# Kernel tuning notes

Hardware: AMD Instinct MI355X
Metric: run time of the kernel (lower is better)

## Reference

```python
import jax, jax.numpy as jnp
import numpy as np

B, T = 32, 64
C, H, W = 1, 32, 32
A, E, D, S, HID = 2, 64, 128, 32, 128
K, STRIDE, PAD = 4, 2, 1
FEAT = 64 * 4 * 4  # conv stack output: 64 channels at 4x4


def _lin(x, w, b):
    return x @ w.T + b


def _conv(x, w, b):
    y = jax.lax.conv_general_dilated(x, w, (STRIDE, STRIDE), [(PAD, PAD)] * 2,
                                     dimension_numbers=('NCHW', 'OIHW', 'NCHW'))
    return y + b[None, :, None, None]


def _deconv(x, w, b):
    # torch ConvTranspose2d(w: (in_c,out_c,k,k), stride=2, pad=1) as dilated conv
    w_ = jnp.flip(w, (2, 3)).transpose(1, 0, 2, 3)
    p = K - 1 - PAD
    y = jax.lax.conv_general_dilated(x, w_, (1, 1), [(p, p)] * 2,
                                     lhs_dilation=(STRIDE, STRIDE),
                                     dimension_numbers=('NCHW', 'OIHW', 'NCHW'))
    return y + b[None, :, None, None]


def _mlp(x, w1, b1, w2, b2, w3, b3):
    h = jax.nn.elu(_lin(x, w1, b1))
    h = jax.nn.elu(_lin(h, w2, b2))
    out = _lin(h, w3, b3)
    return out[..., :S], jnp.clip(out[..., S:], -5.0, 2.0)


def _gru(x, h, wih, whh, bih, bhh):
    # torch nn.GRUCell semantics
    gi = x @ wih.T + bih
    gh = h @ whh.T + bhh
    ir, iz, inn = jnp.split(gi, 3, -1)
    hr, hz, hn = jnp.split(gh, 3, -1)
    r = jax.nn.sigmoid(ir + hr)
    u = jax.nn.sigmoid(iz + hz)
    n = jnp.tanh(inn + r * hn)
    return (1.0 - u) * n + u * h


def setup_inputs():
    keys = iter(jax.random.split(jax.random.key(0), 64))

    def p(shape, fan):
        return jax.random.normal(next(keys), shape, jnp.float32) / np.sqrt(fan)

    return dict(
        obs=jax.random.normal(next(keys), (B, T, C, H, W), jnp.float32),
        actions=jax.random.normal(next(keys), (B, T, A), jnp.float32),
        noise=jax.random.normal(next(keys), (T, B, S), jnp.float32),
        enc_w1=p((32, C, K, K), C * K * K), enc_b1=jnp.zeros(32),
        enc_w2=p((64, 32, K, K), 32 * K * K), enc_b2=jnp.zeros(64),
        enc_w3=p((64, 64, K, K), 64 * K * K), enc_b3=jnp.zeros(64),
        enc_pw=p((E, FEAT), FEAT), enc_pb=jnp.zeros(E),
        dec_pw=p((FEAT, D + S), D + S), dec_pb=jnp.zeros(FEAT),
        dec_w1=p((64, 64, K, K), 64 * K * K), dec_b1=jnp.zeros(64),
        dec_w2=p((64, 32, K, K), 64 * K * K), dec_b2=jnp.zeros(32),
        dec_w3=p((32, C, K, K), 32 * K * K), dec_b3=jnp.zeros(C),
        gru_wih=p((3 * D, S + A), D), gru_whh=p((3 * D, D), D),
        gru_bih=jnp.zeros(3 * D), gru_bhh=jnp.zeros(3 * D),
        pri_w1=p((HID, D + A), D + A), pri_b1=jnp.zeros(HID),
        pri_w2=p((HID, HID), HID), pri_b2=jnp.zeros(HID),
        pri_w3=p((2 * S, HID), HID), pri_b3=jnp.zeros(2 * S),
        pos_w1=p((HID, D + E), D + E), pos_b1=jnp.zeros(HID),
        pos_w2=p((HID, HID), HID), pos_b2=jnp.zeros(HID),
        pos_w3=p((2 * S, HID), HID), pos_b3=jnp.zeros(2 * S),
    )


def reference(obs, actions, noise, enc_w1, enc_b1, enc_w2, enc_b2, enc_w3, enc_b3,
              enc_pw, enc_pb, dec_pw, dec_pb, dec_w1, dec_b1, dec_w2, dec_b2,
              dec_w3, dec_b3, gru_wih, gru_whh, gru_bih, gru_bhh,
              pri_w1, pri_b1, pri_w2, pri_b2, pri_w3, pri_b3,
              pos_w1, pos_b1, pos_w2, pos_b2, pos_w3, pos_b3):
    Bq, Tq = obs.shape[:2]
    # --- CNN encoder over all frames at once ---
    x = obs.reshape(Bq * Tq, C, H, W)
    x = jax.nn.relu(_conv(x, enc_w1, enc_b1))
    x = jax.nn.relu(_conv(x, enc_w2, enc_b2))
    x = jax.nn.relu(_conv(x, enc_w3, enc_b3))
    embed = _lin(x.reshape(Bq * Tq, -1), enc_pw, enc_pb).reshape(Bq, Tq, E)

    # --- sequential RSSM core (use_posterior=True path) ---
    def step(h, inp):
        a, e_t, eps = inp
        pm, pls = _mlp(jnp.concatenate([h, e_t], -1),
                       pos_w1, pos_b1, pos_w2, pos_b2, pos_w3, pos_b3)
        z = pm + jnp.exp(pls) * eps
        prm, prls = _mlp(jnp.concatenate([h, a], -1),
                         pri_w1, pri_b1, pri_w2, pri_b2, pri_w3, pri_b3)
        h_new = _gru(jnp.concatenate([z, a], -1), h, gru_wih, gru_whh, gru_bih, gru_bhh)
        return h_new, (z, prm, prls, pm, pls, h)  # h = pre-update (used for decode)

    h0 = jnp.zeros((Bq, D), obs.dtype)
    h_final, (zs, prm, prls, pm, pls, hs) = jax.lax.scan(
        step, h0, (actions.swapaxes(0, 1), embed.swapaxes(0, 1), noise))

    # --- batched decode of all (h_t, z_t); same math as per-step decode ---
    hz = jnp.concatenate([hs, zs], -1).reshape(Tq * Bq, D + S)
    y = _lin(hz, dec_pw, dec_pb).reshape(Tq * Bq, 64, 4, 4)
    y = jax.nn.relu(_deconv(y, dec_w1, dec_b1))
    y = jax.nn.relu(_deconv(y, dec_w2, dec_b2))
    y = jax.nn.sigmoid(_deconv(y, dec_w3, dec_b3))
    recons = y.reshape(Tq, Bq, C, H, W).swapaxes(0, 1)

    tb = lambda t: t.swapaxes(0, 1)  # (T,B,.) -> (B,T,.)
    return (recons, tb(zs), tb(prm), tb(prls), tb(pm), tb(pls), h_final)
```

## Files before the change

kernel.cpp:

```cpp
#include <hip/hip_runtime.h>
#include <math.h>

#define NB 32
#define NT 64
#define NF 2048

#define OUT_ZS    2097152
#define OUT_PRM   (OUT_ZS + 65536)
#define OUT_PRLS  (OUT_PRM + 65536)
#define OUT_PM    (OUT_PRLS + 65536)
#define OUT_PLS   (OUT_PM + 65536)
#define OUT_HF    (OUT_PLS + 65536)

#define WS_HS    27394048
#define WS_ENCT  27656192
#define WS_DECT  27721728
#define WS_WP1H  27885568
#define WS_WP2   27893760
#define WS_WP3   27901952
#define WS_WWHH  27906048
#define WS_WIHZ  27930624
#define WS_QW1T  27936768
#define WS_QW2T  27953408
#define WS_QW3T  27969792
#define WS_PW1T  27977984
#define WS_WIHT  28002560
#define WS_WC2   16777216
#define WS_WC3   (WS_WC2 + 16384)
#define WS_WD1   (WS_WC3 + 32768)
#define WS_WD2   (WS_WD1 + 32768)
#define WS_POSL1E 25165824
#define WS_GIA    (WS_POSL1E + 262144)

typedef __attribute__((ext_vector_type(8))) short short8;
typedef __attribute__((ext_vector_type(4))) float floatx4;
typedef _Float16 __attribute__((ext_vector_type(2))) half2v;
union U4S8 { uint4 u; short8 s; };
__device__ __forceinline__ short8 u2s(uint4 u) { U4S8 x; x.u = u; return x.s; }
__device__ __forceinline__ float eluf(float a) { return (a > 0.f) ? a : expm1f(a); }
__device__ __forceinline__ float sigm(float a) { return 1.f / (1.f + expf(-a)); }
__device__ __forceinline__ unsigned short f2bf(float f) {
  unsigned int u = __float_as_uint(f);
  u += 0x7fffu + ((u >> 16) & 1u);
  return (unsigned short)(u >> 16);
}
__device__ __forceinline__ unsigned short f2h(float f) {
  _Float16 h = (_Float16)f;
  return __builtin_bit_cast(unsigned short, h);
}
__device__ __forceinline__ float dotp8(uint4 u, const float* __restrict__ x) {
  float4 x0 = *reinterpret_cast<const float4*>(x);
  float4 x1 = *reinterpret_cast<const float4*>(x + 4);
  float acc;
  acc  = __uint_as_float(u.x << 16) * x0.x;
  acc += __uint_as_float(u.x & 0xffff0000u) * x0.y;
  acc += __uint_as_float(u.y << 16) * x0.z;
  acc += __uint_as_float(u.y & 0xffff0000u) * x0.w;
  acc += __uint_as_float(u.z << 16) * x1.x;
  acc += __uint_as_float(u.z & 0xffff0000u) * x1.y;
  acc += __uint_as_float(u.w << 16) * x1.z;
  acc += __uint_as_float(u.w & 0xffff0000u) * x1.w;
  return acc;
}

union U4H2 { uint4 u; half2v h[4]; };
__device__ __forceinline__ void dot8h(uint4 w, uint4 x,
                                      float& a0, float& a1, float& a2, float& a3) {
  U4H2 W; W.u = w;
  U4H2 X; X.u = x;
#if __has_builtin(__builtin_amdgcn_fdot2)
  a0 = __builtin_amdgcn_fdot2(W.h[0], X.h[0], a0, false);
  a1 = __builtin_amdgcn_fdot2(W.h[1], X.h[1], a1, false);
  a2 = __builtin_amdgcn_fdot2(W.h[2], X.h[2], a2, false);
  a3 = __builtin_amdgcn_fdot2(W.h[3], X.h[3], a3, false);
#else
  a0 = fmaf((float)W.h[0][0], (float)X.h[0][0], a0);
  a0 = fmaf((float)W.h[0][1], (float)X.h[0][1], a0);
  a1 = fmaf((float)W.h[1][0], (float)X.h[1][0], a1);
  a1 = fmaf((float)W.h[1][1], (float)X.h[1][1], a1);
  a2 = fmaf((float)W.h[2][0], (float)X.h[2][0], a2);
  a2 = fmaf((float)W.h[2][1], (float)X.h[2][1], a2);
  a3 = fmaf((float)W.h[3][0], (float)X.h[3][0], a3);
  a3 = fmaf((float)W.h[3][1], (float)X.h[3][1], a3);
#endif
}

struct PP { const float* src; void* dst; int n; int mode; int A; int B; };
struct PPAll { PP m[16]; };

__global__ __launch_bounds__(256) void k_prep(PPAll a) {
  PP p = a.m[blockIdx.y];
  for (int i = blockIdx.x * 256 + threadIdx.x; i < p.n; i += gridDim.x * 256) {
    if (p.mode == 10) {
      const int r = i / p.B, c = i - r * p.B;
      ((float*)p.dst)[c * p.A + r] = p.src[i];
    } else {
      float v;
      if (p.mode == 0) v = p.src[i];
      else if (p.mode == 1) v = p.src[(i >> 7) * 192 + (i & 127)];
      else if (p.mode == 2) v = p.src[(i >> 5) * 34 + (i & 31)];
      else {
        const int ab = p.A * p.B;
        const int t = i / ab, rem = i - t * ab;
        const int oc = rem / p.B, ic = rem - oc * p.B;
        v = (p.mode == 3) ? p.src[(oc * p.B + ic) * 16 + t]
                          : p.src[(ic * p.A + oc) * 16 + t];
      }
      ((unsigned short*)p.dst)[i] = (p.mode <= 2) ? f2h(v) : f2bf(v);
    }
  }
}

__global__ __launch_bounds__(256, 2) void k_enc(
    const float* __restrict__ obs, const float* __restrict__ act,
    const float* __restrict__ w1, const float* __restrict__ b1,
    const unsigned short* __restrict__ wc2, const float* __restrict__ b2,
    const unsigned short* __restrict__ wc3, const float* __restrict__ b3,
    const float* __restrict__ encT, const float* __restrict__ encb,
    const float* __restrict__ pw1T, const float* __restrict__ pb1,
    const float* __restrict__ wihT, const float* __restrict__ bih,
    float* __restrict__ posl1e, float* __restrict__ gia) {
  const int f = blockIdx.x, tid = threadIdx.x;
  const int w = tid >> 6, l = tid & 63, q = l >> 4, n = l & 15;
  __shared__ float sIn1[32 * 33];
  __shared__ float sW1[512];
  __shared__ float sB1[32];
  __shared__ __align__(16) unsigned short sIn2[18 * 18 * 40];
  __shared__ __align__(16) unsigned short sIn3[10 * 10 * 72];
  __shared__ __align__(16) float sXe[1024];
  __shared__ float sP[256];
  __shared__ float sE[64];
  __shared__ float sA2[2];

  {
    const float* in = obs + (size_t)f * 1024;
    for (int i = tid; i < 1024; i += 256) sIn1[(i >> 5) * 33 + (i & 31)] = in[i];
    for (int i = tid; i < 512; i += 256) sW1[i] = w1[i];
    if (tid < 32) sB1[tid] = b1[tid];
    if (tid < 2) sA2[tid] = act[(size_t)f * 2 + tid];
    unsigned int* z2 = (unsigned int*)sIn2;
    for (int i = tid; i < 18 * 18 * 40 / 2; i += 256) z2[i] = 0u;
    unsigned int* z3 = (unsigned int*)sIn3;
    for (int i = tid; i < 10 * 10 * 72 / 2; i += 256) z3[i] = 0u;
  }
  __syncthreads();
  for (int r = tid; r < 512; r += 256) {
    const int oc = r >> 4, oy = r & 15;
    float acc[16];
    const float bv = sB1[oc];
#pragma unroll
    for (int j = 0; j < 16; j++) acc[j] = bv;
#pragma unroll
    for (int ky = 0; ky < 4; ky++) {
      const int iy = 2 * oy + ky - 1;
      if (iy < 0 || iy >= 32) continue;
#pragma unroll
      for (int kx = 0; kx < 4; kx++) {
        const float wv = sW1[oc * 16 + ky * 4 + kx];
#pragma unroll
        for (int j = 0; j < 16; j++) {
          const int ix = 2 * j + kx - 1;
          if (ix >= 0 && ix < 32) acc[j] += wv * sIn1[iy * 33 + ix];
        }
      }
    }
#pragma unroll
    for (int j = 0; j < 16; j++)
      sIn2[((oy + 1) * 18 + (j + 1)) * 40 + oc] = f2bf(fmaxf(acc[j], 0.f));
  }
  __syncthreads();
  {
    int base[4];
#pragma unroll
    for (int nt = 0; nt < 4; nt++) {
      const int px = nt * 16 + n, oy = px >> 3, ox = px & 7;
      base[nt] = ((2 * oy + 1) * 18 + (2 * ox + 1)) * 40 + q * 8;
    }
    floatx4 acc[4];
#pragma unroll
    for (int nt = 0; nt < 4; nt++) acc[nt] = (floatx4){0.f, 0.f, 0.f, 0.f};
    uint4 af[16];
#pragma unroll
    for (int t = 0; t < 16; t++)
      af[t] = *reinterpret_cast<const uint4*>(wc2 + (size_t)(t * 64 + w * 16 + n) * 32 + q * 8);
#pragma unroll
    for (int t = 0; t < 16; t++) {
      const int toff = ((t / 4 - 1) * 18 + (t % 4 - 1)) * 40;
#pragma unroll
      for (int nt = 0; nt < 4; nt++) {
        uint4 bf = *reinterpret_cast<const uint4*>(&sIn2[base[nt] + toff]);
        acc[nt] = __builtin_amdgcn_mfma_f32_16x16x32_bf16(u2s(af[t]), u2s(bf), acc[nt], 0, 0, 0);
      }
    }
    float b4[4];
#pragma unroll
    for (int r = 0; r < 4; r++) b4[r] = b2[w * 16 + q * 4 + r];
    __syncthreads();
#pragma unroll
    for (int nt = 0; nt < 4; nt++) {
      const int px = nt * 16 + n, oy = px >> 3, ox = px & 7;
#pragma unroll
      for (int r = 0; r < 4; r++)
        sIn3[((oy + 1) * 10 + (ox + 1)) * 72 + (w * 16 + q * 4 + r)] =
            f2bf(fmaxf(acc[nt][r] + b4[r], 0.f));
    }
  }
  __syncthreads();
  {
    const int oy = n >> 2, ox = n & 3;
    const int ibase = ((2 * oy + 1) * 10 + (2 * ox + 1)) * 72 + q * 8;
    floatx4 acc = (floatx4){0.f, 0.f, 0.f, 0.f};
    for (int ks = 0; ks < 2; ks++) {
      uint4 af[16];
#pragma unroll
      for (int t = 0; t < 16; t++)
        af[t] = *reinterpret_cast<const uint4*>(
            wc3 + (size_t)(t * 64 + w * 16 + n) * 64 + ks * 32 + q * 8);
#pragma unroll
      for (int t = 0; t < 16; t++) {
        const int toff = ((t / 4 - 1) * 10 + (t % 4 - 1)) * 72 + ks * 32;
        uint4 bf = *reinterpret_cast<const uint4*>(&sIn3[ibase + toff]);
        acc = __builtin_amdgcn_mfma_f32_16x16x32_bf16(u2s(af[t]), u2s(bf), acc, 0, 0, 0);
      }
    }
#pragma unroll
    for (int r = 0; r < 4; r++) {
      const int ch = w * 16 + q * 4 + r;
      sXe[ch * 16 + n] = fmaxf(acc[r] + b3[ch], 0.f);
    }
  }
  __syncthreads();
  {
    const int o = tid & 63, s = tid >> 6;
    float acc = 0.f;
    const int k0 = s * 256;
    for (int k = k0; k < k0 + 256; k++) acc += encT[k * 64 + o] * sXe[k];
    sP[tid] = acc;
  }
  __syncthreads();
  if (tid < 64)
    sE[tid] = sP[tid] + sP[tid + 64] + sP[tid + 128] + sP[tid + 192] + encb[tid];
  __syncthreads();
  if (tid < 128) {
    float a = pb1[tid];
    for (int k = 0; k < 64; k++) a += pw1T[(128 + k) * 128 + tid] * sE[k];
    posl1e[(size_t)f * 128 + tid] = a;
  } else {
#pragma unroll
    for (int jj = 0; jj < 3; jj++) {
      const int j = (tid - 128) + jj * 128;
      gia[(size_t)f * 384 + j] =
          bih[j] + wihT[32 * 384 + j] * sA2[0] + wihT[33 * 384 + j] * sA2[1];
    }
  }
}

__global__ __launch_bounds__(512, 2) void k_rssm4(
    const float* __restrict__ posl1e, const float* __restrict__ gia,
    const float* __restrict__ noise,
    const unsigned short* __restrict__ wp1h, const unsigned short* __restrict__ wp2,
    const unsigned short* __restrict__ wp3, const unsigned short* __restrict__ wwhh,
    const unsigned short* __restrict__ wihz,
    const float* __restrict__ pb2, const float* __restrict__ pb3,
    const float* __restrict__ bhh,
    float* __restrict__ hs, float* __restrict__ out) {
  const int b = blockIdx.x, tid = threadIdx.x;
  __shared__ __align__(16) _Float16 sHh[128];
  __shared__ __align__(16) _Float16 sL1h[128];
  __shared__ __align__(16) _Float16 sL2h[128];
  __shared__ __align__(16) _Float16 sZh[32];
  __shared__ float sGh[384];
  __shared__ float sPM[64];

  uint4 wA[16];
  {
    const unsigned short* rowA =
        (tid < 128) ? (wp1h + tid * 128) : (wwhh + (size_t)(tid - 128) * 128);
#pragma unroll
    for (int i = 0; i < 16; i++) wA[i] = reinterpret_cast<const uint4*>(rowA)[i];
  }
  uint4 wB[4];
  {
    const unsigned short* rowB = wp2 + (tid >> 2) * 128 + (tid & 3) * 32;
#pragma unroll
    for (int i = 0; i < 4; i++) wB[i] = reinterpret_cast<const uint4*>(rowB)[i];
  }
  uint4 wC[2];
  {
    const unsigned short* rowC = wp3 + (tid >> 3) * 128 + (tid & 7) * 16;
#pragma unroll
    for (int i = 0; i < 2; i++) wC[i] = reinterpret_cast<const uint4*>(rowC)[i];
  }
  uint4 wD[3][4];
  if (tid < 128) {
#pragma unroll
    for (int j = 0; j < 3; j++) {
      const unsigned short* rowD = wihz + (size_t)(tid + 128 * j) * 32;
#pragma unroll
      for (int i = 0; i < 4; i++) wD[j][i] = reinterpret_cast<const uint4*>(rowD)[i];
    }
  }
  const float bhhR = (tid >= 128) ? bhh[tid - 128] : 0.f;
  const float pb2R = pb2[tid >> 2];
  const float pb3mR = (tid < 32) ? pb3[tid] : 0.f;
  const float pb3sR = (tid < 32) ? pb3[tid + 32] : 0.f;

  float h_reg = 0.f;
  float pl1R = 0.f, gaR0 = 0.f, gaR1 = 0.f, gaR2 = 0.f, epsR = 0.f;
  if (tid < 128) {
    pl1R = posl1e[(size_t)(b * 64) * 128 + tid];
    const size_t gb = (size_t)(b * 64) * 384 + tid;
    gaR0 = gia[gb];
    gaR1 = gia[gb + 128];
    gaR2 = gia[gb + 256];
    sHh[tid] = (_Float16)0.f;
    hs[(size_t)b * 128 + tid] = 0.f;
  }
  if (tid < 32) epsR = noise[(size_t)b * 32 + tid];
  __syncthreads();

  for (int t = 0; t < 64; ++t) {
    const int tn = (t < 63) ? t + 1 : 63;
    float pl1N = 0.f, gaN0 = 0.f, gaN1 = 0.f, gaN2 = 0.f, epsN = 0.f;
    if (tid < 128) {
      pl1N = posl1e[(size_t)(b * 64 + tn) * 128 + tid];
      const size_t gb = (size_t)(b * 64 + tn) * 384 + tid;
      gaN0 = gia[gb];
      gaN1 = gia[gb + 128];
      gaN2 = gia[gb + 256];
    }
    if (tid < 32) epsN = noise[(size_t)(tn * 32 + b) * 32 + tid];

    {
      float a0 = 0.f, a1 = 0.f, a2 = 0.f, a3 = 0.f;
      const uint4* xs = reinterpret_cast<const uint4*>(sHh);
#pragma unroll
      for (int g = 0; g < 16; g++) dot8h(wA[g], xs[g], a0, a1, a2, a3);
      const float a = (a0 + a1) + (a2 + a3);
      if (tid < 128) sL1h[tid] = (_Float16)eluf(a + pl1R);
      else sGh[tid - 128] = a + bhhR;
    }
    __syncthreads();
    {
      float a0 = 0.f, a1 = 0.f, a2 = 0.f, a3 = 0.f;
      const uint4* xs = reinterpret_cast<const uint4*>(sL1h) + (tid & 3) * 4;
#pragma unroll
      for (int i = 0; i < 4; i++) dot8h(wB[i], xs[i], a0, a1, a2, a3);
      float p = (a0 + a1) + (a2 + a3);
      p += __shfl_xor(p, 1);
      p += __shfl_xor(p, 2);
      if ((tid & 3) == 0) sL2h[tid >> 2] = (_Float16)eluf(p + pb2R);
    }
    __syncthreads();
    {
      float a0 = 0.f, a1 = 0.f, a2 = 0.f, a3 = 0.f;
      const uint4* xs = reinterpret_cast<const uint4*>(sL2h) + (tid & 7) * 2;
      dot8h(wC[0], xs[0], a0, a1, a2, a3);
      dot8h(wC[1], xs[1], a0, a1, a2, a3);
      float p = (a0 + a1) + (a2 + a3);
      p += __shfl_xor(p, 1);
      p += __shfl_xor(p, 2);
      p += __shfl_xor(p, 4);
      if ((tid & 7) == 0) sPM[tid >> 3] = p;
    }
    __syncthreads();
    if (tid < 32) {
      const float pm = sPM[tid] + pb3mR;
      float pls = sPM[32 + tid] + pb3sR;
      pls = fminf(fmaxf(pls, -5.f), 2.f);
      const float z = pm + expf(pls) * epsR;
      sZh[tid] = (_Float16)z;
      const int o = (b * 64 + t) * 32 + tid;
      out[OUT_ZS + o] = z;
      out[OUT_PM + o] = pm;
      out[OUT_PLS + o] = pls;
    }
    __syncthreads();
    if (tid < 128) {
      float r0 = 0.f, r1 = 0.f, r2 = 0.f, r3 = 0.f;
      float u0 = 0.f, u1 = 0.f, u2 = 0.f, u3 = 0.f;
      float m0 = 0.f, m1 = 0.f, m2 = 0.f, m3 = 0.f;
      const uint4* xs = reinterpret_cast<const uint4*>(sZh);
#pragma unroll
      for (int i = 0; i < 4; i++) {
        const uint4 xv = xs[i];
        dot8h(wD[0][i], xv, r0, r1, r2, r3);
        dot8h(wD[1][i], xv, u0, u1, u2, u3);
        dot8h(wD[2][i], xv, m0, m1, m2, m3);
      }
      const float gr = gaR0 + ((r0 + r1) + (r2 + r3));
      const float gu = gaR1 + ((u0 + u1) + (u2 + u3));
      const float gn = gaR2 + ((m0 + m1) + (m2 + m3));
      const float r = sigm(gr + sGh[tid]);
      const float u = sigm(gu + sGh[128 + tid]);
      const float n = tanhf(gn + r * sGh[256 + tid]);
      const float hn = (1.f - u) * n + u * h_reg;
      h_reg = hn;
      sHh[tid] = (_Float16)hn;
      if (t < 63) hs[(size_t)((t + 1) * 32 + b) * 128 + tid] = hn;
    }
    pl1R = pl1N;
    gaR0 = gaN0;
    gaR1 = gaN1;
    gaR2 = gaN2;
    epsR = epsN;
    __syncthreads();
  }
  if (tid < 128) out[OUT_HF + b * 128 + tid] = h_reg;
}

__global__ __launch_bounds__(128) void k_pri(const float* __restrict__ hs,
    const float* __restrict__ act,
    const float* __restrict__ qw1T, const float* __restrict__ qb1,
    const float* __restrict__ qw2T, const float* __restrict__ qb2,
    const float* __restrict__ qw3T, const float* __restrict__ qb3,
    float* __restrict__ out) {
  __shared__ float sV[128], sW[128];
  __shared__ float sA2[2];
  const int f = blockIdx.x, tid = threadIdx.x;
  const int t = f >> 5, b = f & 31;
  sV[tid] = hs[(size_t)f * 128 + tid];
  if (tid < 2) sA2[tid] = act[(size_t)(b * 64 + t) * 2 + tid];
  __syncthreads();
  {
    float a = qb1[tid];
    for (int k = 0; k < 128; k++) a += qw1T[k * 128 + tid] * sV[k];
    a += qw1T[128 * 128 + tid] * sA2[0] + qw1T[129 * 128 + tid] * sA2[1];
    sW[tid] = eluf(a);
  }
  __syncthreads();
  {
    float a = qb2[tid];
    for (int k = 0; k < 128; k++) a += qw2T[k * 128 + tid] * sW[k];
    sV[tid] = eluf(a);
  }
  __syncthreads();
  if (tid < 64) {
    float a = qb3[tid];
    for (int k = 0; k < 128; k++) a += qw3T[k * 64 + tid] * sV[k];
    const int o = (b * 64 + t) * 32;
    if (tid < 32) out[OUT_PRM + o + tid] = a;
    else out[OUT_PRLS + o + tid - 32] = fminf(fmaxf(a, -5.f), 2.f);
  }
}

__global__ __launch_bounds__(256, 2) void k_dec(
    const float* __restrict__ hs, const float* __restrict__ zs,
    const float* __restrict__ decT, const float* __restrict__ decb,
    const unsigned short* __restrict__ wd1, const float* __restrict__ db1,
    const unsigned short* __restrict__ wd2, const float* __restrict__ db2,
    const float* __restrict__ w3, const float* __restrict__ b3,
    float* __restrict__ out) {
  const int f = blockIdx.x, tid = threadIdx.x;
  const int w = tid >> 6, l = tid & 63, q = l >> 4, n = l & 15;
  const int t = f >> 5, b = f & 31;
  __shared__ float sX[160];
  __shared__ __align__(16) unsigned short sInD1[6 * 6 * 72];
  __shared__ __align__(16) unsigned short sInD2[10 * 10 * 72];
  __shared__ float sInD3[32 * 16 * 17];
  __shared__ float sW3[32 * 16 * 2];

  if (tid < 128) sX[tid] = hs[(size_t)f * 128 + tid];
  else if (tid < 160) sX[tid] = zs[(size_t)(b * 64 + t) * 32 + (tid - 128)];
  {
    unsigned int* z1 = (unsigned int*)sInD1;
    for (int i = tid; i < 6 * 6 * 72 / 2; i += 256) z1[i] = 0u;
    unsigned int* z2 = (unsigned int*)sInD2;
    for (int i = tid; i < 10 * 10 * 72 / 2; i += 256) z2[i] = 0u;
    for (int s = tid; s < 512; s += 256) {
      const int icc = s >> 4, tap = s & 15;
      sW3[(icc * 16 + tap) * 2] = w3[s];
    }
  }
  __syncthreads();
  {
    float acc[4];
#pragma unroll
    for (int i = 0; i < 4; i++) acc[i] = decb[i * 256 + tid];
    for (int k = 0; k < 160; k++) {
      const float xv = sX[k];
#pragma unroll
      for (int i = 0; i < 4; i++) acc[i] += decT[k * 1024 + i * 256 + tid] * xv;
    }
#pragma unroll
    for (int i = 0; i < 4; i++) {
      const int o = i * 256 + tid, c = o >> 4, px = o & 15;
      const int Y = px >> 2, X = px & 3;
      sInD1[((Y + 1) * 6 + (X + 1)) * 72 + c] = f2bf(acc[i]);
    }
  }
  __syncthreads();
  {
    const int Y = n >> 2, X = n & 3;
    const int ibase = ((Y + 1) * 6 + (X + 1)) * 72 + q * 8;
    float b4[4];
#pragma unroll
    for (int r = 0; r < 4; r++) b4[r] = db1[w * 16 + q * 4 + r];
#pragma unroll
    for (int c = 0; c < 4; c++) {
      const int cy = c >> 1, cx = c & 1;
      floatx4 acc = (floatx4){0.f, 0.f, 0.f, 0.f};
      for (int ks = 0; ks < 2; ks++) {
        uint4 af[4];
#pragma unroll
        for (int tt = 0; tt < 4; tt++) {
          const int t2 = tt >> 1, t3 = tt & 1;
          const int ky = ((cy + 1) & 1) + 2 * t2, kx = ((cx + 1) & 1) + 2 * t3;
          af[tt] = *reinterpret_cast<const uint4*>(
              wd1 + (size_t)((ky * 4 + kx) * 64 + w * 16 + n) * 64 + ks * 32 + q * 8);
        }
#pragma unroll
        for (int tt = 0; tt < 4; tt++) {
          const int t2 = tt >> 1, t3 = tt & 1;
          const int toff = ((cy - t2) * 6 + (cx - t3)) * 72 + ks * 32;
          uint4 bf = *reinterpret_cast<const uint4*>(&sInD1[ibase + toff]);
          acc = __builtin_amdgcn_mfma_f32_16x16x32_bf16(u2s(af[tt]), u2s(bf), acc, 0, 0, 0);
        }
      }
      const int oy = 2 * Y + cy, ox = 2 * X + cx;
#pragma unroll
      for (int r = 0; r < 4; r++)
        sInD2[((oy + 1) * 10 + (ox + 1)) * 72 + (w * 16 + q * 4 + r)] =
            f2bf(fmaxf(acc[r] + b4[r], 0.f));
    }
  }
  __syncthreads();
  {
    const int px = w * 16 + n;
    const int Y = px >> 3, X = px & 7;
    const int ibase = ((Y + 1) * 10 + (X + 1)) * 72 + q * 8;
    float b4[2][4];
#pragma unroll
    for (int mi = 0; mi < 2; mi++)
#pragma unroll
      for (int r = 0; r < 4; r++) b4[mi][r] = db2[mi * 16 + q * 4 + r];
#pragma unroll
    for (int c = 0; c < 4; c++) {
      const int cy = c >> 1, cx = c & 1;
      floatx4 acc[2];
      acc[0] = (floatx4){0.f, 0.f, 0.f, 0.f};
      acc[1] = (floatx4){0.f, 0.f, 0.f, 0.f};
      for (int ks = 0; ks < 2; ks++) {
        uint4 af[2][4];
#pragma unroll
        for (int mi = 0; mi < 2; mi++)
#pragma unroll
          for (int tt = 0; tt < 4; tt++) {
            const int t2 = tt >> 1, t3 = tt & 1;
            const int ky = ((cy + 1) & 1) + 2 * t2, kx = ((cx + 1) & 1) + 2 * t3;
            af[mi][tt] = *reinterpret_cast<const uint4*>(
                wd2 + (size_t)((ky * 4 + kx) * 32 + mi * 16 + n) * 64 + ks * 32 + q * 8);
          }
#pragma unroll
        for (int tt = 0; tt < 4; tt++) {
          const int t2 = tt >> 1, t3 = tt & 1;
          const int toff = ((cy - t2) * 10 + (cx - t3)) * 72 + ks * 32;
          uint4 bf = *reinterpret_cast<const uint4*>(&sInD2[ibase + toff]);
#pragma unroll
          for (int mi = 0; mi < 2; mi++)
            acc[mi] = __builtin_amdgcn_mfma_f32_16x16x32_bf16(u2s(af[mi][tt]), u2s(bf),
                                                              acc[mi], 0, 0, 0);
        }
      }
      const int oy = 2 * Y + cy, ox = 2 * X + cx;
#pragma unroll
      for (int mi = 0; mi < 2; mi++)
#pragma unroll
        for (int r = 0; r < 4; r++) {
          const int oc = mi * 16 + q * 4 + r;
          sInD3[oc * 272 + oy * 17 + ox] = fmaxf(acc[mi][r] + b4[mi][r], 0.f);
        }
    }
  }
  __syncthreads();
  {
    const int oy = tid >> 3;
    const int rem2 = tid & 7;
    const int cpar = rem2 >> 2, qq = rem2 & 3;
    const int py = (oy + 1) & 1, pc = (cpar + 1) & 1;
    float acc[4];
    const float bv = b3[0];
#pragma unroll
    for (int j = 0; j < 4; j++) acc[j] = bv;
    for (int icc = 0; icc < 32; icc++) {
      const float* inb = &sInD3[icc * 272];
      const float* wb = &sW3[icc * 32];
#pragma unroll
      for (int t2 = 0; t2 < 2; t2++) {
        const int ky = py + 2 * t2;
        const int iy = (oy + 1 - ky) >> 1;
        if (iy < 0 || iy >= 16) continue;
        const float* row = inb + iy * 17;
#pragma unroll
        for (int t3 = 0; t3 < 2; t3++) {
          const int kx = pc + 2 * t3;
          const int ixb = (cpar + 1 - kx) >> 1;
          const float wv = wb[(ky * 4 + kx) * 2];
#pragma unroll
          for (int j = 0; j < 4; j++) {
            const int ix = ixb + qq * 4 + j;
            if (ix >= 0 && ix < 16) acc[j] += wv * row[ix];
          }
        }
      }
    }
    const int fo = b * 64 + t;
    float* yf = out + (size_t)fo * 1024;
#pragma unroll
    for (int j = 0; j < 4; j++)
      yf[oy * 32 + (cpar + 2 * (qq * 4 + j))] = 1.f / (1.f + expf(-acc[j]));
  }
}

extern "C" void kernel_launch(void* const* d_in, const int* in_sizes, int n_in,
                              void* d_out, int out_size, void* d_ws, size_t ws_size,
                              hipStream_t stream) {
  const float* obs = (const float*)d_in[0];
  const float* actions = (const float*)d_in[1];
  const float* noise = (const float*)d_in[2];
  const float* enc_w1 = (const float*)d_in[3];
  const float* enc_b1 = (const float*)d_in[4];
  const float* enc_w2 = (const float*)d_in[5];
  const float* enc_b2 = (const float*)d_in[6];
  const float* enc_w3 = (const float*)d_in[7];
  const float* enc_b3 = (const float*)d_in[8];
  const float* enc_pw = (const float*)d_in[9];
  const float* enc_pb = (const float*)d_in[10];
  const float* dec_pw = (const float*)d_in[11];
  const float* dec_pb = (const float*)d_in[12];
  const float* dec_w1 = (const float*)d_in[13];
  const float* dec_b1 = (const float*)d_in[14];
  const float* dec_w2 = (const float*)d_in[15];
  const float* dec_b2 = (const float*)d_in[16];
  const float* dec_w3 = (const float*)d_in[17];
  const float* dec_b3 = (const float*)d_in[18];
  const float* gru_wih = (const float*)d_in[19];
  const float* gru_whh = (const float*)d_in[20];
  const float* gru_bih = (const float*)d_in[21];
  const float* gru_bhh = (const float*)d_in[22];
  const float* pri_w1 = (const float*)d_in[23];
  const float* pri_b1 = (const float*)d_in[24];
  const float* pri_w2 = (const float*)d_in[25];
  const float* pri_b2 = (const float*)d_in[26];
  const float* pri_w3 = (const float*)d_in[27];
  const float* pri_b3 = (const float*)d_in[28];
  const float* pos_w1 = (const float*)d_in[29];
  const float* pos_b1 = (const float*)d_in[30];
  const float* pos_w2 = (const float*)d_in[31];
  const float* pos_b2 = (const float*)d_in[32];
  const float* pos_w3 = (const float*)d_in[33];
  const float* pos_b3 = (const float*)d_in[34];

  float* out = (float*)d_out;
  float* ws = (float*)d_ws;
  float* HS = ws + WS_HS;
  float* POSL1E = ws + WS_POSL1E;
  float* GIA = ws + WS_GIA;
  unsigned short* WP1H = (unsigned short*)(ws + WS_WP1H);
  unsigned short* WP2 = (unsigned short*)(ws + WS_WP2);
  unsigned short* WP3 = (unsigned short*)(ws + WS_WP3);
  unsigned short* WWHH = (unsigned short*)(ws + WS_WWHH);
  unsigned short* WIHZ = (unsigned short*)(ws + WS_WIHZ);
  unsigned short* WC2 = (unsigned short*)(ws + WS_WC2);
  unsigned short* WC3 = (unsigned short*)(ws + WS_WC3);
  unsigned short* WD1 = (unsigned short*)(ws + WS_WD1);
  unsigned short* WD2 = (unsigned short*)(ws + WS_WD2);

  PPAll pp;
  pp.m[0]  = {enc_pw, ws + WS_ENCT, 64 * 1024, 10, 64, 1024};
  pp.m[1]  = {dec_pw, ws + WS_DECT, 1024 * 160, 10, 1024, 160};
  pp.m[2]  = {pri_w1, ws + WS_QW1T, 128 * 130, 10, 128, 130};
  pp.m[3]  = {pri_w2, ws + WS_QW2T, 128 * 128, 10, 128, 128};
  pp.m[4]  = {pri_w3, ws + WS_QW3T, 64 * 128, 10, 64, 128};
  pp.m[5]  = {pos_w1, ws + WS_PW1T, 128 * 192, 10, 128, 192};
  pp.m[6]  = {gru_wih, ws + WS_WIHT, 384 * 34, 10, 384, 34};
  pp.m[7]  = {pos_w1, WP1H, 128 * 128, 1, 0, 0};
  pp.m[8]  = {pos_w2, WP2, 128 * 128, 0, 0, 0};
  pp.m[9]  = {pos_w3, WP3, 64 * 128, 0, 0, 0};
  pp.m[10] = {gru_whh, WWHH, 384 * 128, 0, 0, 0};
  pp.m[11] = {gru_wih, WIHZ, 384 * 32, 2, 0, 0};
  pp.m[12] = {enc_w2, WC2, 16 * 64 * 32, 3, 64, 32};
  pp.m[13] = {enc_w3, WC3, 16 * 64 * 64, 3, 64, 64};
  pp.m[14] = {dec_w1, WD1, 16 * 64 * 64, 4, 64, 64};
  pp.m[15] = {dec_w2, WD2, 16 * 32 * 64, 4, 32, 64};
  hipLaunchKernelGGL(k_prep, dim3(32, 16), dim3(256), 0, stream, pp);

  k_enc<<<NF, 256, 0, stream>>>(obs, actions, enc_w1, enc_b1, WC2, enc_b2,
                                WC3, enc_b3, ws + WS_ENCT, enc_pb,
                                ws + WS_PW1T, pos_b1, ws + WS_WIHT, gru_bih,
                                POSL1E, GIA);

  k_rssm4<<<NB, 512, 0, stream>>>(POSL1E, GIA, noise, WP1H, WP2, WP3, WWHH, WIHZ,
                                  pos_b2, pos_b3, gru_bhh, HS, out);
  k_pri<<<NF, 128, 0, stream>>>(HS, actions, ws + WS_QW1T, pri_b1,
                                ws + WS_QW2T, pri_b2, ws + WS_QW3T, pri_b3, out);

  k_dec<<<NF, 256, 0, stream>>>(HS, out + OUT_ZS, ws + WS_DECT, dec_pb,
                                WD1, dec_b1, WD2, dec_b2, dec_w3, dec_b3, out);
}
```

Baseline: 508.7 us.

## Use fp16 packed dot products in decoder projection and final deconv

The decoder's dense projection now reads fp16 weights, repacked by the prep kernel into a k-quad interleaved layout, and uses fdot2 instead of fp32 FMAs. The final deconvolution stores its input activations and weights in fp16, channel-innermost, in shared memory and computes with dot8h. This cuts shared memory use and lets launch bounds ask for 4 blocks per SM instead of 2. It lowers global and LDS bandwidth per block and raises occupancy, at the cost of fp16 rounding of activations and weights.

```diff
diff --git a/kernel.cpp b/kernel.cpp
--- a/kernel.cpp
+++ b/kernel.cpp
@@ -48,19 +48,15 @@
   _Float16 h = (_Float16)f;
   return __builtin_bit_cast(unsigned short, h);
 }
-__device__ __forceinline__ float dotp8(uint4 u, const float* __restrict__ x) {
-  float4 x0 = *reinterpret_cast<const float4*>(x);
-  float4 x1 = *reinterpret_cast<const float4*>(x + 4);
-  float acc;
-  acc  = __uint_as_float(u.x << 16) * x0.x;
-  acc += __uint_as_float(u.x & 0xffff0000u) * x0.y;
-  acc += __uint_as_float(u.y << 16) * x0.z;
-  acc += __uint_as_float(u.y & 0xffff0000u) * x0.w;
-  acc += __uint_as_float(u.z << 16) * x1.x;
-  acc += __uint_as_float(u.z & 0xffff0000u) * x1.y;
-  acc += __uint_as_float(u.w << 16) * x1.z;
-  acc += __uint_as_float(u.w & 0xffff0000u) * x1.w;
-  return acc;
+union UH2 { unsigned int u; half2v h; };
+__device__ __forceinline__ half2v u2h(unsigned int u) { UH2 x; x.u = u; return x.h; }
+
+__device__ __forceinline__ float fdot2w(half2v a, half2v b, float c) {
+#if __has_builtin(__builtin_amdgcn_fdot2)
+  return __builtin_amdgcn_fdot2(a, b, c, false);
+#else
+  return fmaf((float)a[0], (float)b[0], fmaf((float)a[1], (float)b[1], c));
+#endif
 }
 
 union U4H2 { uint4 u; half2v h[4]; };
@@ -68,21 +64,10 @@
                                       float& a0, float& a1, float& a2, float& a3) {
   U4H2 W; W.u = w;
   U4H2 X; X.u = x;
-#if __has_builtin(__builtin_amdgcn_fdot2)
-  a0 = __builtin_amdgcn_fdot2(W.h[0], X.h[0], a0, false);
-  a1 = __builtin_amdgcn_fdot2(W.h[1], X.h[1], a1, false);
-  a2 = __builtin_amdgcn_fdot2(W.h[2], X.h[2], a2, false);
-  a3 = __builtin_amdgcn_fdot2(W.h[3], X.h[3], a3, false);
-#else
-  a0 = fmaf((float)W.h[0][0], (float)X.h[0][0], a0);
-  a0 = fmaf((float)W.h[0][1], (float)X.h[0][1], a0);
-  a1 = fmaf((float)W.h[1][0], (float)X.h[1][0], a1);
-  a1 = fmaf((float)W.h[1][1], (float)X.h[1][1], a1);
-  a2 = fmaf((float)W.h[2][0], (float)X.h[2][0], a2);
-  a2 = fmaf((float)W.h[2][1], (float)X.h[2][1], a2);
-  a3 = fmaf((float)W.h[3][0], (float)X.h[3][0], a3);
-  a3 = fmaf((float)W.h[3][1], (float)X.h[3][1], a3);
-#endif
+  a0 = fdot2w(W.h[0], X.h[0], a0);
+  a1 = fdot2w(W.h[1], X.h[1], a1);
+  a2 = fdot2w(W.h[2], X.h[2], a2);
+  a3 = fdot2w(W.h[3], X.h[3], a3);
 }
 
 struct PP { const float* src; void* dst; int n; int mode; int A; int B; };
@@ -99,14 +84,17 @@
       if (p.mode == 0) v = p.src[i];
       else if (p.mode == 1) v = p.src[(i >> 7) * 192 + (i & 127)];
       else if (p.mode == 2) v = p.src[(i >> 5) * 34 + (i & 31)];
-      else {
+      else if (p.mode == 5) {
+        const int kq = i >> 12, o = (i >> 2) & 1023, kl = (i >> 1) & 1, h = i & 1;
+        v = p.src[o * 160 + kq * 4 + kl * 2 + h];
+      } else {
         const int ab = p.A * p.B;
         const int t = i / ab, rem = i - t * ab;
         const int oc = rem / p.B, ic = rem - oc * p.B;
         v = (p.mode == 3) ? p.src[(oc * p.B + ic) * 16 + t]
                           : p.src[(ic * p.A + oc) * 16 + t];
       }
-      ((unsigned short*)p.dst)[i] = (p.mode <= 2) ? f2h(v) : f2bf(v);
+      ((unsigned short*)p.dst)[i] = (p.mode <= 2 || p.mode == 5) ? f2h(v) : f2bf(v);
     }
   }
 }
@@ -444,9 +432,9 @@
   }
 }
 
-__global__ __launch_bounds__(256, 2) void k_dec(
+__global__ __launch_bounds__(256, 4) void k_dec(
     const float* __restrict__ hs, const float* __restrict__ zs,
-    const float* __restrict__ decT, const float* __restrict__ decb,
+    const unsigned short* __restrict__ decTh, const float* __restrict__ decb,
     const unsigned short* __restrict__ wd1, const float* __restrict__ db1,
     const unsigned short* __restrict__ wd2, const float* __restrict__ db2,
     const float* __restrict__ w3, const float* __restrict__ b3,
@@ -454,39 +442,46 @@
   const int f = blockIdx.x, tid = threadIdx.x;
   const int w = tid >> 6, l = tid & 63, q = l >> 4, n = l & 15;
   const int t = f >> 5, b = f & 31;
-  __shared__ float sX[160];
+  __shared__ __align__(16) _Float16 sXh[160];
   __shared__ __align__(16) unsigned short sInD1[6 * 6 * 72];
   __shared__ __align__(16) unsigned short sInD2[10 * 10 * 72];
-  __shared__ float sInD3[32 * 16 * 17];
-  __shared__ float sW3[32 * 16 * 2];
-
-  if (tid < 128) sX[tid] = hs[(size_t)f * 128 + tid];
-  else if (tid < 160) sX[tid] = zs[(size_t)(b * 64 + t) * 32 + (tid - 128)];
+  __shared__ __align__(16) _Float16 sInD3h[16 * 16 * 32];
+  __shared__ __align__(16) _Float16 sW3h[16 * 32];
+
+  if (tid < 128) sXh[tid] = (_Float16)hs[(size_t)f * 128 + tid];
+  else if (tid < 160) sXh[tid] = (_Float16)zs[(size_t)(b * 64 + t) * 32 + (tid - 128)];
   {
     unsigned int* z1 = (unsigned int*)sInD1;
     for (int i = tid; i < 6 * 6 * 72 / 2; i += 256) z1[i] = 0u;
     unsigned int* z2 = (unsigned int*)sInD2;
     for (int i = tid; i < 10 * 10 * 72 / 2; i += 256) z2[i] = 0u;
     for (int s = tid; s < 512; s += 256) {
-      const int icc = s >> 4, tap = s & 15;
-      sW3[(icc * 16 + tap) * 2] = w3[s];
-    }
-  }
-  __syncthreads();
-  {
-    float acc[4];
-#pragma unroll
-    for (int i = 0; i < 4; i++) acc[i] = decb[i * 256 + tid];
-    for (int k = 0; k < 160; k++) {
-      const float xv = sX[k];
-#pragma unroll
-      for (int i = 0; i < 4; i++) acc[i] += decT[k * 1024 + i * 256 + tid] * xv;
+      const int tap = s >> 5, icc = s & 31;
+      sW3h[s] = (_Float16)w3[icc * 16 + tap];
+    }
+  }
+  __syncthreads();
+  {
+    float acA[4] = {0.f, 0.f, 0.f, 0.f};
+    float acB[4] = {0.f, 0.f, 0.f, 0.f};
+    const uint2* dT = reinterpret_cast<const uint2*>(decTh);
+    const unsigned int* xh = reinterpret_cast<const unsigned int*>(sXh);
+#pragma unroll 2
+    for (int kq = 0; kq < 40; kq++) {
+      const half2v x0 = u2h(xh[2 * kq]);
+      const half2v x1 = u2h(xh[2 * kq + 1]);
+#pragma unroll
+      for (int i = 0; i < 4; i++) {
+        const uint2 wv = dT[kq * 1024 + i * 256 + tid];
+        acA[i] = fdot2w(u2h(wv.x), x0, acA[i]);
+        acB[i] = fdot2w(u2h(wv.y), x1, acB[i]);
+      }
     }
 #pragma unroll
     for (int i = 0; i < 4; i++) {
       const int o = i * 256 + tid, c = o >> 4, px = o & 15;
       const int Y = px >> 2, X = px & 3;
-      sInD1[((Y + 1) * 6 + (X + 1)) * 72 + c] = f2bf(acc[i]);
+      sInD1[((Y + 1) * 6 + (X + 1)) * 72 + c] = f2bf(acA[i] + acB[i] + decb[o]);
     }
   }
   __syncthreads();
@@ -564,12 +559,16 @@
       }
       const int oy = 2 * Y + cy, ox = 2 * X + cx;
 #pragma unroll
-      for (int mi = 0; mi < 2; mi++)
-#pragma unroll
-        for (int r = 0; r < 4; r++) {
-          const int oc = mi * 16 + q * 4 + r;
-          sInD3[oc * 272 + oy * 17 + ox] = fmaxf(acc[mi][r] + b4[mi][r], 0.f);
-        }
+      for (int mi = 0; mi < 2; mi++) {
+        const unsigned int lo =
+            (unsigned int)f2h(fmaxf(acc[mi][0] + b4[mi][0], 0.f)) |
+            ((unsigned int)f2h(fmaxf(acc[mi][1] + b4[mi][1], 0.f)) << 16);
+        const unsigned int hi =
+            (unsigned int)f2h(fmaxf(acc[mi][2] + b4[mi][2], 0.f)) |
+            ((unsigned int)f2h(fmaxf(acc[mi][3] + b4[mi][3], 0.f)) << 16);
+        *reinterpret_cast<uint2*>(&sInD3h[(oy * 16 + ox) * 32 + mi * 16 + q * 4]) =
+            make_uint2(lo, hi);
+      }
     }
   }
   __syncthreads();
@@ -578,29 +577,30 @@
     const int rem2 = tid & 7;
     const int cpar = rem2 >> 2, qq = rem2 & 3;
     const int py = (oy + 1) & 1, pc = (cpar + 1) & 1;
-    float acc[4];
+    float acc[4] = {0.f, 0.f, 0.f, 0.f};
     const float bv = b3[0];
 #pragma unroll
-    for (int j = 0; j < 4; j++) acc[j] = bv;
-    for (int icc = 0; icc < 32; icc++) {
-      const float* inb = &sInD3[icc * 272];
-      const float* wb = &sW3[icc * 32];
-#pragma unroll
-      for (int t2 = 0; t2 < 2; t2++) {
-        const int ky = py + 2 * t2;
-        const int iy = (oy + 1 - ky) >> 1;
-        if (iy < 0 || iy >= 16) continue;
-        const float* row = inb + iy * 17;
-#pragma unroll
-        for (int t3 = 0; t3 < 2; t3++) {
-          const int kx = pc + 2 * t3;
-          const int ixb = (cpar + 1 - kx) >> 1;
-          const float wv = wb[(ky * 4 + kx) * 2];
-#pragma unroll
-          for (int j = 0; j < 4; j++) {
-            const int ix = ixb + qq * 4 + j;
-            if (ix >= 0 && ix < 16) acc[j] += wv * row[ix];
-          }
+    for (int u2 = 0; u2 < 2; u2++) {
+      const int ky = py + 2 * u2;
+      const int iy = (oy + 1 - ky) >> 1;
+      if (iy < 0 || iy >= 16) continue;
+#pragma unroll
+      for (int u3 = 0; u3 < 2; u3++) {
+        const int kx = pc + 2 * u3;
+        const int ixb = (cpar + 1 - kx) >> 1;
+        const uint4* wv = reinterpret_cast<const uint4*>(&sW3h[(ky * 4 + kx) * 32]);
+        const uint4 w0 = wv[0], w1 = wv[1], w2 = wv[2], w3v = wv[3];
+#pragma unroll
+        for (int j = 0; j < 4; j++) {
+          const int ix = ixb + qq * 4 + j;
+          if (ix < 0 || ix >= 16) continue;
+          const uint4* xp = reinterpret_cast<const uint4*>(&sInD3h[(iy * 16 + ix) * 32]);
+          float a0 = 0.f, a1 = 0.f, a2 = 0.f, a3 = 0.f;
+          dot8h(w0, xp[0], a0, a1, a2, a3);
+          dot8h(w1, xp[1], a0, a1, a2, a3);
+          dot8h(w2, xp[2], a0, a1, a2, a3);
+          dot8h(w3v, xp[3], a0, a1, a2, a3);
+          acc[j] += (a0 + a1) + (a2 + a3);
         }
       }
     }
@@ -608,7 +608,7 @@
     float* yf = out + (size_t)fo * 1024;
 #pragma unroll
     for (int j = 0; j < 4; j++)
-      yf[oy * 32 + (cpar + 2 * (qq * 4 + j))] = 1.f / (1.f + expf(-acc[j]));
+      yf[oy * 32 + (cpar + 2 * (qq * 4 + j))] = 1.f / (1.f + expf(-(acc[j] + bv)));
   }
 }
 
@@ -665,10 +665,11 @@
   unsigned short* WC3 = (unsigned short*)(ws + WS_WC3);
   unsigned short* WD1 = (unsigned short*)(ws + WS_WD1);
   unsigned short* WD2 = (unsigned short*)(ws + WS_WD2);
+  unsigned short* DECTH = (unsigned short*)(ws + WS_DECT);
 
   PPAll pp;
   pp.m[0]  = {enc_pw, ws + WS_ENCT, 64 * 1024, 10, 64, 1024};
-  pp.m[1]  = {dec_pw, ws + WS_DECT, 1024 * 160, 10, 1024, 160};
+  pp.m[1]  = {dec_pw, DECTH, 160 * 1024, 5, 0, 0};
   pp.m[2]  = {pri_w1, ws + WS_QW1T, 128 * 130, 10, 128, 130};
   pp.m[3]  = {pri_w2, ws + WS_QW2T, 128 * 128, 10, 128, 128};
   pp.m[4]  = {pri_w3, ws + WS_QW3T, 64 * 128, 10, 64, 128};
@@ -695,6 +696,6 @@
   k_pri<<<NF, 128, 0, stream>>>(HS, actions, ws + WS_QW1T, pri_b1,
                                 ws + WS_QW2T, pri_b2, ws + WS_QW3T, pri_b3, out);
 
-  k_dec<<<NF, 256, 0, stream>>>(HS, out + OUT_ZS, ws + WS_DECT, dec_pb,
+  k_dec<<<NF, 256, 0, stream>>>(HS, out + OUT_ZS, DECTH, dec_pb,
                                 WD1, dec_b1, WD2, dec_b2, dec_w3, dec_b3, out);
 }
```

Measured after the change: 481.0 us. -5.4%, faster.
